# Performance work log

Hardware: AMD Instinct MI355X
Metric: run time of the kernel (lower is better)

## Reference

```python
import jax, jax.numpy as jnp
import numpy as np

B, T, IN, H, OUT = 32, 2048, 256, 512, 256
DT = 0.1


def _orthogonal(key, n):
    a = jax.random.normal(key, (n, n), dtype=jnp.float32)
    q, r = jnp.linalg.qr(a)
    return q * jnp.sign(jnp.diag(r))[None, :]


def _xavier(key, fan_out, fan_in):
    bound = np.sqrt(6.0 / (fan_in + fan_out)).astype(np.float32)
    return jax.random.uniform(key, (fan_out, fan_in), minval=-bound, maxval=bound, dtype=jnp.float32)


def setup_inputs() -> dict:
    key = jax.random.key(0)
    ks = jax.random.split(key, 9)
    x = jax.random.normal(ks[0], (B, T, IN), dtype=jnp.float32)
    W_in0 = _xavier(ks[1], H, IN)
    b_in0 = jnp.zeros((H,), dtype=jnp.float32)
    W_rec0 = _orthogonal(ks[2], H)
    tau0 = jnp.clip(jax.random.uniform(ks[3], (H,), minval=0.5, maxval=2.0, dtype=jnp.float32), 0.1, 10.0)
    W_in1 = _xavier(ks[4], H, H)
    b_in1 = jnp.zeros((H,), dtype=jnp.float32)
    W_rec1 = _orthogonal(ks[5], H)
    tau1 = jnp.clip(jax.random.uniform(ks[6], (H,), minval=0.5, maxval=2.0, dtype=jnp.float32), 0.1, 10.0)
    bound = np.sqrt(1.0 / H).astype(np.float32)
    W_out = jax.random.uniform(ks[7], (OUT, H), minval=-bound, maxval=bound, dtype=jnp.float32)
    b_out = jax.random.uniform(ks[8], (OUT,), minval=-bound, maxval=bound, dtype=jnp.float32)
    return {"x": x, "W_in0": W_in0, "b_in0": b_in0, "W_rec0": W_rec0, "tau0": tau0,
            "W_in1": W_in1, "b_in1": b_in1, "W_rec1": W_rec1, "tau1": tau1,
            "W_out": W_out, "b_out": b_out}


def _cell(x_t, h, W_in, b_in, W_rec, tau):
    # CT-RNN Euler step: h + dt * (act(W_in x + W_rec h) - h) / clamp(tau)
    tau_c = jnp.clip(tau, 0.1, 10.0)
    target = jnp.tanh(x_t @ W_in.T + b_in + h @ W_rec.T)
    return h + DT * (target - h) / tau_c


def reference(x, W_in0, b_in0, W_rec0, tau0, W_in1, b_in1, W_rec1, tau1, W_out, b_out):
    def step(carry, x_t):
        h0, h1 = carry
        h0 = _cell(x_t, h0, W_in0, b_in0, W_rec0, tau0)
        h1 = _cell(h0, h1, W_in1, b_in1, W_rec1, tau1)
        out_t = h1 @ W_out.T + b_out  # [B, OUT]
        return (h0, h1), out_t

    h0 = jnp.zeros((x.shape[0], H), dtype=x.dtype)
    h1 = jnp.zeros((x.shape[0], H), dtype=x.dtype)
    xs = jnp.swapaxes(x, 0, 1)  # [T, B, IN]
    _, outs = jax.lax.scan(step, (h0, h1), xs)
    out = jnp.swapaxes(outs, 0, 1)  # [B, T, OUT]
    return out + x  # use_residual since input_size == output_size
```

## Files before the change

kernel.cpp:

```cpp
#include <hip/hip_runtime.h>
#include <cstdint>
#include <cstddef>

typedef __attribute__((ext_vector_type(8))) short short8;
typedef __attribute__((ext_vector_type(4))) short short4v;
typedef __attribute__((ext_vector_type(4))) float f32x4;

#define TT 2048
#define BB 32
#define HH 512

__device__ inline short f2bf(float f) {
  union { float f; unsigned u; } v; v.f = f;
  unsigned r = v.u + 0x7fffu + ((v.u >> 16) & 1u);
  return (short)(r >> 16);
}
__device__ inline float bf2f(short s) {
  union { unsigned u; float f; } v; v.u = ((unsigned)(unsigned short)s) << 16;
  return v.f;
}

__device__ inline void barrier_lds() {
  asm volatile("s_waitcnt lgkmcnt(0)\n\ts_barrier" ::: "memory");
}


__global__ void convert_weights(const float* __restrict__ w0, const float* __restrict__ w1,
                                const float* __restrict__ w2, const float* __restrict__ w3,
                                const float* __restrict__ w4, short* __restrict__ dst) {
  int i = blockIdx.x * 256 + threadIdx.x;
  if (i >= 1048576) return;
  const float* src; int off;
  if (i < 131072)      { src = w0; off = i; }
  else if (i < 393216) { src = w1; off = i - 131072; }
  else if (i < 655360) { src = w2; off = i - 393216; }
  else if (i < 917504) { src = w3; off = i - 655360; }
  else                 { src = w4; off = i - 917504; }
  dst[i] = f2bf(src[off]);
}

template<int A_XF32, int OUT_SW, int RESID>
__global__ __launch_bounds__(256) void gemm_bt(const void* __restrict__ Ap,
    const short* __restrict__ Bw, const float* __restrict__ bias,
    const float* __restrict__ resid, void* __restrict__ Cp, int M, int N, int K) {
  __shared__ short As[64][40];
  __shared__ short Bs[64][40];
  int tid = threadIdx.x;
  int m0 = blockIdx.x * 64, n0 = blockIdx.y * 64;
  int w = tid >> 6, lane = tid & 63;
  int wm = w >> 1, wn = w & 1;
  int quad = lane >> 4, l16 = lane & 15;
  f32x4 acc[2][2];
#pragma unroll
  for (int i = 0; i < 2; i++)
#pragma unroll
    for (int j = 0; j < 2; j++) acc[i][j] = (f32x4){0.f, 0.f, 0.f, 0.f};
  int lr = tid >> 2, lk = (tid & 3) * 8;
  for (int kk = 0; kk < K; kk += 32) {
    __syncthreads();
    {
      int rl = m0 + lr;
      if (A_XF32) {
        const float* A = (const float*)Ap;
        size_t phys = ((size_t)(rl & 31) * TT + (rl >> 5)) * K;
        const float4* p = (const float4*)(A + phys + kk + lk);
        float4 a0 = p[0], a1 = p[1];
        short8 v;
        v[0] = f2bf(a0.x); v[1] = f2bf(a0.y); v[2] = f2bf(a0.z); v[3] = f2bf(a0.w);
        v[4] = f2bf(a1.x); v[5] = f2bf(a1.y); v[6] = f2bf(a1.z); v[7] = f2bf(a1.w);
        *(short8*)&As[lr][lk] = v;
      } else {
        const short* A = (const short*)Ap;
        *(short8*)&As[lr][lk] = *(const short8*)(A + (size_t)rl * K + kk + lk);
      }
      *(short8*)&Bs[lr][lk] = *(const short8*)(Bw + (size_t)(n0 + lr) * K + kk + lk);
    }
    __syncthreads();
    short8 af[2], bfr[2];
#pragma unroll
    for (int i = 0; i < 2; i++) af[i] = *(short8*)&As[wm * 32 + i * 16 + l16][quad * 8];
#pragma unroll
    for (int j = 0; j < 2; j++) bfr[j] = *(short8*)&Bs[wn * 32 + j * 16 + l16][quad * 8];
#pragma unroll
    for (int i = 0; i < 2; i++)
#pragma unroll
      for (int j = 0; j < 2; j++)
        acc[i][j] = __builtin_amdgcn_mfma_f32_16x16x32_bf16(af[i], bfr[j], acc[i][j], 0, 0, 0);
  }
#pragma unroll
  for (int i = 0; i < 2; i++) {
#pragma unroll
    for (int j = 0; j < 2; j++) {
#pragma unroll
      for (int rr = 0; rr < 4; rr++) {
        int row = m0 + wm * 32 + i * 16 + quad * 4 + rr;
        int col = n0 + wn * 32 + j * 16 + l16;
        float v2 = acc[i][j][rr] + bias[col];
        if (OUT_SW) {
          int t = row >> 5, b = row & 31;
          int wg2 = b >> 4, bl = b & 15;
          int wv2 = col >> 6, ct2 = (col >> 4) & 3, q2 = (col >> 2) & 3, r2 = col & 3;
          size_t idx = (((((size_t)t * 2 + wg2) * 8 + wv2) * 4 + ct2) * 64 + (q2 * 16 + bl)) * 4 + r2;
          ((short*)Cp)[idx] = f2bf(v2);
        } else {
          size_t idx = ((size_t)(row & 31) * TT + (row >> 5)) * N + col;
          if (RESID) v2 += resid[idx];
          ((float*)Cp)[idx] = v2;
        }
      }
    }
  }
}

__global__ __launch_bounds__(512, 2) void seq_scan(
    const short* __restrict__ xin_sw, const short* __restrict__ Wrec,
    const float* __restrict__ tau, short* __restrict__ hall) {
  __shared__ short Wl[8][16][64][8];
  __shared__ __align__(16) short hb[16][520];
  int wg = blockIdx.x;
  int tid = threadIdx.x;
  int wv = tid >> 6, lane = tid & 63;
  int q = lane >> 4, l16 = lane & 15;
  int c0 = wv * 64;

  for (int i = tid; i < 16 * 520 / 2; i += 512) ((int*)hb)[i] = 0;

  short8 wreg[48];
#pragma unroll
  for (int ct = 0; ct < 4; ct++) {
    const short* wrow = Wrec + (size_t)(c0 + ct * 16 + l16) * HH;
#pragma unroll
    for (int kc = 0; kc < 12; kc++)
      wreg[ct * 12 + kc] = *(const short8*)(wrow + kc * 32 + q * 8);
#pragma unroll
    for (int kc = 12; kc < 16; kc++)
      *(short8*)&Wl[wv][ct * 4 + (kc - 12)][lane][0] = *(const short8*)(wrow + kc * 32 + q * 8);
  }
  float rate[16];
#pragma unroll
  for (int ct = 0; ct < 4; ct++)
#pragma unroll
    for (int r = 0; r < 4; r++) {
      float tc = tau[c0 + ct * 16 + q * 4 + r];
      tc = fminf(fmaxf(tc, 0.1f), 10.f);
      rate[ct * 4 + r] = 0.1f / tc;
    }
  float st[16];
#pragma unroll
  for (int i = 0; i < 16; i++) st[i] = 0.f;

  const short* xbase = xin_sw + (size_t)wg * 8192 + wv * 1024 + lane * 4;
  short* hallp = hall + ((size_t)wg * 16 + l16) * HH + c0 + q * 4;

  short4v xrA[4], xrB[4];
#pragma unroll
  for (int ct = 0; ct < 4; ct++) xrA[ct] = *(const short4v*)(xbase + ct * 256);
  __syncthreads();

#define STEP_BODY(T, XU, XP)                                                      \
  {                                                                               \
    int tn = ((T) + 1 < TT) ? (T) + 1 : (T);                                      \
    const short* xp_ = xbase + (size_t)tn * 16384;                                \
    _Pragma("unroll")                                                             \
    for (int ct = 0; ct < 4; ct++) XP[ct] = *(const short4v*)(xp_ + ct * 256);    \
    f32x4 acc[4];                                                                 \
    _Pragma("unroll")                                                             \
    for (int ct = 0; ct < 4; ct++) acc[ct] = (f32x4){0.f, 0.f, 0.f, 0.f};         \
    _Pragma("unroll")                                                             \
    for (int kc = 0; kc < 12; kc++) {                                             \
      short8 af = *(short8*)&hb[l16][kc * 32 + q * 8];                            \
      _Pragma("unroll")                                                           \
      for (int ct = 0; ct < 4; ct++)                                              \
        acc[ct] = __builtin_amdgcn_mfma_f32_16x16x32_bf16(wreg[ct * 12 + kc],     \
                                                          af, acc[ct], 0, 0, 0);  \
    }                                                                             \
    _Pragma("unroll")                                                             \
    for (int kc = 12; kc < 16; kc++) {                                            \
      short8 af = *(short8*)&hb[l16][kc * 32 + q * 8];                            \
      _Pragma("unroll")                                                           \
      for (int ct = 0; ct < 4; ct++) {                                            \
        short8 wf = *(short8*)&Wl[wv][ct * 4 + (kc - 12)][lane][0];               \
        acc[ct] = __builtin_amdgcn_mfma_f32_16x16x32_bf16(wf, af, acc[ct], 0, 0, 0); \
      }                                                                           \
    }                                                                             \
    barrier_lds();                                 \
    short* hp_ = hallp + ((size_t)(T) * 32) * HH;                                 \
    _Pragma("unroll")                                                             \
    for (int ct = 0; ct < 4; ct++) {                                              \
      short4v hv;                                                                 \
      _Pragma("unroll")                                                           \
      for (int r = 0; r < 4; r++) {                                               \
        float u = acc[ct][r] + bf2f(XU[ct][r]);                                   \
        float v = u * 2.8853900817779268f;                                        \
        v = fminf(fmaxf(v, -30.f), 30.f);                                         \
        float e = __builtin_amdgcn_exp2f(v);                                      \
        float tg = (e - 1.f) * __builtin_amdgcn_rcpf(e + 1.f);                    \
        float h = st[ct * 4 + r];                                                 \
        h += rate[ct * 4 + r] * (tg - h);                                         \
        st[ct * 4 + r] = h;                                                       \
        hv[r] = f2bf(h);                                                          \
      }                                                                           \
      *(short4v*)&hb[l16][c0 + ct * 16 + q * 4] = hv;                             \
      *(short4v*)(hp_ + ct * 16) = hv;                                            \
    }                                                                             \
    barrier_lds();                                          \
  }

  for (int t = 0; t < TT; t += 2) {
    STEP_BODY(t, xrA, xrB);
    STEP_BODY(t + 1, xrB, xrA);
  }
#undef STEP_BODY
}

extern "C" void kernel_launch(void* const* d_in, const int* in_sizes, int n_in,
                              void* d_out, int out_size, void* d_ws, size_t ws_size,
                              hipStream_t stream) {
  const float* x      = (const float*)d_in[0];
  const float* W_in0  = (const float*)d_in[1];
  const float* b_in0  = (const float*)d_in[2];
  const float* W_rec0 = (const float*)d_in[3];
  const float* tau0   = (const float*)d_in[4];
  const float* W_in1  = (const float*)d_in[5];
  const float* b_in1  = (const float*)d_in[6];
  const float* W_rec1 = (const float*)d_in[7];
  const float* tau1   = (const float*)d_in[8];
  const float* W_out  = (const float*)d_in[9];
  const float* b_out  = (const float*)d_in[10];

  char* ws = (char*)d_ws;
  short* wb     = (short*)ws;
  short* xin_sw = (short*)(ws + (4u << 20));
  short* hall   = (short*)(ws + (68u << 20));

  short* wbin0  = wb;
  short* wbrec0 = wb + 131072;
  short* wbin1  = wb + 393216;
  short* wbrec1 = wb + 655360;
  short* wbout  = wb + 917504;

  convert_weights<<<4096, 256, 0, stream>>>(W_in0, W_rec0, W_in1, W_rec1, W_out, wb);

  dim3 g1(1024, 8);
  gemm_bt<1, 1, 0><<<g1, 256, 0, stream>>>((const void*)x, wbin0, b_in0, nullptr,
                                           (void*)xin_sw, BB * TT, HH, 256);
  seq_scan<<<2, 512, 0, stream>>>(xin_sw, wbrec0, tau0, hall);
  gemm_bt<0, 1, 0><<<g1, 256, 0, stream>>>((const void*)hall, wbin1, b_in1, nullptr,
                                           (void*)xin_sw, BB * TT, HH, HH);
  seq_scan<<<2, 512, 0, stream>>>(xin_sw, wbrec1, tau1, hall);
  dim3 g2(1024, 4);
  gemm_bt<0, 0, 1><<<g2, 256, 0, stream>>>((const void*)hall, wbout, b_out, x,
                                           d_out, BB * TT, 256, HH);
}
```

Measured before the change: 14.03 ms.

## Fuse both recurrent scans and the middle GEMM into one pipelined persistent kernel

Replaces the sequential launches (layer-0 scan, layer-1 input GEMM, layer-1 scan) with one persistent kernel. Two blocks run the layer-0 scan, two run the layer-1 scan, and 64 helper blocks compute the layer-1 input projection in 32-step chunks. Progress is passed between them through global flags with acquire/release atomics. The intent is to overlap the two serial recurrences so the layer-1 scan trails layer-0 by about one chunk instead of waiting for it to finish. The cost is spin-waiting, flag traffic, and the assumption that all 68 blocks are co-resident. It also relies on careful reuse of the shared xin_sw and hall buffers between layers.

```diff
diff --git a/kernel.cpp b/kernel.cpp
--- a/kernel.cpp
+++ b/kernel.cpp
@@ -9,6 +9,9 @@
 #define TT 2048
 #define BB 32
 #define HH 512
+#define CH 32
+#define NCHUNK (TT / CH)
+#define NHELP 64
 
 __device__ inline short f2bf(float f) {
   union { float f; unsigned u; } v; v.f = f;
@@ -112,13 +115,94 @@
   }
 }
 
-__global__ __launch_bounds__(512, 2) void seq_scan(
-    const short* __restrict__ xin_sw, const short* __restrict__ Wrec,
-    const float* __restrict__ tau, short* __restrict__ hall) {
+__global__ __launch_bounds__(512, 2) void fused_pipeline(
+    short* __restrict__ xin_sw, const short* __restrict__ Wrec0,
+    const float* __restrict__ tau0, const short* __restrict__ Wrec1,
+    const float* __restrict__ tau1, const short* __restrict__ Win1,
+    const float* __restrict__ bin1, short* __restrict__ hall,
+    unsigned* __restrict__ flags) {
   __shared__ short Wl[8][16][64][8];
   __shared__ __align__(16) short hb[16][520];
-  int wg = blockIdx.x;
+  unsigned* done1 = flags + 16;
+  int bid = blockIdx.x;
   int tid = threadIdx.x;
+
+  if (bid >= 4) {
+    int hw = bid - 4;
+    int mt = hw >> 3, nt = hw & 7;
+    short (*As)[40] = (short (*)[40])(&Wl[0][0][0][0]);
+    short (*Bs)[40] = (short (*)[40])(&Wl[0][0][0][0] + 128 * 40);
+    int w = tid >> 6, lane = tid & 63;
+    int wm = w >> 1, wn = w & 1;
+    int quad = lane >> 4, l16 = lane & 15;
+    int lr = tid >> 2, lk = (tid & 3) * 8;
+#pragma unroll 1
+    for (int c = 0; c < NCHUNK; ++c) {
+      unsigned want = (unsigned)(c + 1);
+      if (tid == 0) {
+        while (__hip_atomic_load(&flags[0], __ATOMIC_RELAXED, __HIP_MEMORY_SCOPE_AGENT) < want ||
+               __hip_atomic_load(&flags[1], __ATOMIC_RELAXED, __HIP_MEMORY_SCOPE_AGENT) < want)
+          __builtin_amdgcn_s_sleep(32);
+      }
+      __syncthreads();
+      {
+        unsigned f0 = __hip_atomic_load(&flags[0], __ATOMIC_ACQUIRE, __HIP_MEMORY_SCOPE_AGENT);
+        asm volatile("" :: "v"(f0));
+      }
+      int m0 = c * (CH * 32) + mt * 128;
+      int n0 = nt * 64;
+      f32x4 acc[2][2];
+#pragma unroll
+      for (int i = 0; i < 2; i++)
+#pragma unroll
+        for (int j = 0; j < 2; j++) acc[i][j] = (f32x4){0.f, 0.f, 0.f, 0.f};
+      for (int kk = 0; kk < HH; kk += 32) {
+        __syncthreads();
+        *(short8*)&As[lr][lk] = *(const short8*)(hall + (size_t)(m0 + lr) * HH + kk + lk);
+        if (tid < 256)
+          *(short8*)&Bs[tid >> 2][lk] = *(const short8*)(Win1 + (size_t)(n0 + (tid >> 2)) * HH + kk + lk);
+        __syncthreads();
+        short8 af[2], bfr[2];
+#pragma unroll
+        for (int i = 0; i < 2; i++) af[i] = *(short8*)&As[wm * 32 + i * 16 + l16][quad * 8];
+#pragma unroll
+        for (int j = 0; j < 2; j++) bfr[j] = *(short8*)&Bs[wn * 32 + j * 16 + l16][quad * 8];
+#pragma unroll
+        for (int i = 0; i < 2; i++)
+#pragma unroll
+          for (int j = 0; j < 2; j++)
+            acc[i][j] = __builtin_amdgcn_mfma_f32_16x16x32_bf16(af[i], bfr[j], acc[i][j], 0, 0, 0);
+      }
+#pragma unroll
+      for (int i = 0; i < 2; i++) {
+#pragma unroll
+        for (int j = 0; j < 2; j++) {
+#pragma unroll
+          for (int rr = 0; rr < 4; rr++) {
+            int row = m0 + wm * 32 + i * 16 + quad * 4 + rr;
+            int col = n0 + wn * 32 + j * 16 + l16;
+            float v2 = acc[i][j][rr] + bin1[col];
+            int t = row >> 5, b = row & 31;
+            int wg2 = b >> 4, bl = b & 15;
+            int wv2 = col >> 6, ct2 = (col >> 4) & 3, q2 = (col >> 2) & 3, r2 = col & 3;
+            size_t idx = (((((size_t)t * 2 + wg2) * 8 + wv2) * 4 + ct2) * 64 + (q2 * 16 + bl)) * 4 + r2;
+            xin_sw[idx] = f2bf(v2);
+          }
+        }
+      }
+      asm volatile("s_waitcnt vmcnt(0)" ::: "memory");
+      __syncthreads();
+      if (tid == 0)
+        __hip_atomic_fetch_add(&done1[c], 1u, __ATOMIC_RELEASE, __HIP_MEMORY_SCOPE_AGENT);
+    }
+    return;
+  }
+
+  int producer = (bid < 2);
+  int wg = bid & 1;
+  const short* Wrec = producer ? Wrec0 : Wrec1;
+  const float* taup = producer ? tau0 : tau1;
+
   int wv = tid >> 6, lane = tid & 63;
   int q = lane >> 4, l16 = lane & 15;
   int c0 = wv * 64;
@@ -141,7 +225,7 @@
   for (int ct = 0; ct < 4; ct++)
 #pragma unroll
     for (int r = 0; r < 4; r++) {
-      float tc = tau[c0 + ct * 16 + q * 4 + r];
+      float tc = taup[c0 + ct * 16 + q * 4 + r];
       tc = fminf(fmaxf(tc, 0.1f), 10.f);
       rate[ct * 4 + r] = 0.1f / tc;
     }
@@ -153,8 +237,6 @@
   short* hallp = hall + ((size_t)wg * 16 + l16) * HH + c0 + q * 4;
 
   short4v xrA[4], xrB[4];
-#pragma unroll
-  for (int ct = 0; ct < 4; ct++) xrA[ct] = *(const short4v*)(xbase + ct * 256);
   __syncthreads();
 
 #define STEP_BODY(T, XU, XP)                                                      \
@@ -206,9 +288,36 @@
     barrier_lds();                                          \
   }
 
-  for (int t = 0; t < TT; t += 2) {
-    STEP_BODY(t, xrA, xrB);
-    STEP_BODY(t + 1, xrB, xrA);
+#pragma unroll 1
+  for (int c = 0; c < NCHUNK; ++c) {
+    if (!producer) {
+      int tgt = (c + 1 < NCHUNK) ? (c + 1) : (NCHUNK - 1);
+      if (tid == 0) {
+        while (__hip_atomic_load(&done1[tgt], __ATOMIC_RELAXED, __HIP_MEMORY_SCOPE_AGENT) < (unsigned)NHELP)
+          __builtin_amdgcn_s_sleep(8);
+      }
+      __syncthreads();
+      {
+        unsigned f0 = __hip_atomic_load(&done1[tgt], __ATOMIC_ACQUIRE, __HIP_MEMORY_SCOPE_AGENT);
+        asm volatile("" :: "v"(f0));
+      }
+    }
+    if (c == 0) {
+#pragma unroll
+      for (int ct = 0; ct < 4; ct++) xrA[ct] = *(const short4v*)(xbase + ct * 256);
+    }
+    int tb = c * CH;
+#pragma unroll 1
+    for (int tt = 0; tt < CH; tt += 2) {
+      STEP_BODY(tb + tt, xrA, xrB);
+      STEP_BODY(tb + tt + 1, xrB, xrA);
+    }
+    if (producer) {
+      asm volatile("s_waitcnt vmcnt(0)" ::: "memory");
+      __syncthreads();
+      if (tid == 0)
+        __hip_atomic_store(&flags[wg], (unsigned)(c + 1), __ATOMIC_RELEASE, __HIP_MEMORY_SCOPE_AGENT);
+    }
   }
 #undef STEP_BODY
 }
@@ -230,6 +339,7 @@
 
   char* ws = (char*)d_ws;
   short* wb     = (short*)ws;
+  unsigned* flags = (unsigned*)(ws + (2u << 20));
   short* xin_sw = (short*)(ws + (4u << 20));
   short* hall   = (short*)(ws + (68u << 20));
 
@@ -240,14 +350,15 @@
   short* wbout  = wb + 917504;
 
   convert_weights<<<4096, 256, 0, stream>>>(W_in0, W_rec0, W_in1, W_rec1, W_out, wb);
+  hipMemsetAsync(flags, 0, 1024, stream);
 
   dim3 g1(1024, 8);
   gemm_bt<1, 1, 0><<<g1, 256, 0, stream>>>((const void*)x, wbin0, b_in0, nullptr,
                                            (void*)xin_sw, BB * TT, HH, 256);
-  seq_scan<<<2, 512, 0, stream>>>(xin_sw, wbrec0, tau0, hall);
-  gemm_bt<0, 1, 0><<<g1, 256, 0, stream>>>((const void*)hall, wbin1, b_in1, nullptr,
-                                           (void*)xin_sw, BB * TT, HH, HH);
-  seq_scan<<<2, 512, 0, stream>>>(xin_sw, wbrec1, tau1, hall);
+
+  fused_pipeline<<<4 + NHELP, 512, 0, stream>>>(xin_sw, wbrec0, tau0, wbrec1, tau1,
+                                                wbin1, b_in1, hall, flags);
+
   dim3 g2(1024, 4);
   gemm_bt<0, 0, 1><<<g2, 256, 0, stream>>>((const void*)hall, wbout, b_out, x,
                                            d_out, BB * TT, 256, HH);
```

Result: slower. 17.99 ms (+28.2%).
